# Kernel tuning notes

Measured on AMD Instinct MI355X. Metric: run time of the kernel, lower is better.

The kernel has to match this reference:

```python
import jax, jax.numpy as jnp
import numpy as np
from jax.scipy.special import logsumexp

L = 15      # DATA_MAX_SEG_LEN
K = 64      # XCRIBE_DIM
H = 16      # SEG_DIM
TAG = 32    # TAG_DIM
DUR = 4     # DURATION_DIM
NY = 15     # len(LABELS)
N = 16384   # sequence length
S = 2048    # number of gold segments
NEG = jnp.float32(-1e30)


def setup_inputs() -> dict:
    key = jax.random.key(0)
    ks = jax.random.split(key, 24)
    sL = 1.0 / np.sqrt(H)
    sV = 1.0 / np.sqrt(2 * H + TAG + DUR)
    sW = 1.0 / np.sqrt(H)

    def U(k, shape, s):
        return jax.random.uniform(k, shape, jnp.float32, -s, s)

    return dict(
        data=jax.random.normal(ks[0], (N, K), jnp.float32),
        fwd_Wih=U(ks[1], (4 * H, K), sL), fwd_Whh=U(ks[2], (4 * H, H), sL),
        fwd_bih=U(ks[3], (4 * H,), sL), fwd_bhh=U(ks[4], (4 * H,), sL),
        bwd_Wih=U(ks[5], (4 * H, K), sL), bwd_Whh=U(ks[6], (4 * H, H), sL),
        bwd_bih=U(ks[7], (4 * H,), sL), bwd_bhh=U(ks[8], (4 * H,), sL),
        fwd_h0=jax.random.normal(ks[9], (H,), jnp.float32),
        fwd_c0=jax.random.normal(ks[10], (H,), jnp.float32),
        bwd_h0=jax.random.normal(ks[11], (H,), jnp.float32),
        bwd_c0=jax.random.normal(ks[12], (H,), jnp.float32),
        Y_enc=jax.random.normal(ks[13], (NY, TAG), jnp.float32),
        Z_enc=jax.random.normal(ks[14], (L, DUR), jnp.float32),
        V_W=U(ks[15], (H, 2 * H + TAG + DUR), sV), V_b=U(ks[16], (H,), sV),
        W_W=U(ks[17], (1, H), sW), W_b=U(ks[18], (1,), sW),
        tags=jax.random.randint(ks[19], (S,), 0, NY),
        lengths=jax.random.randint(ks[20], (S,), 1, L + 1),
    )


def _lstm(xs, Wih, Whh, bih, bhh, h0, c0):
    # xs: [L, B, K] -> hidden outputs [L, B, H]; torch gate order i,f,g,o
    B = xs.shape[1]
    b = bih + bhh

    def step(carry, x):
        h, c = carry
        g = x @ Wih.T + h @ Whh.T + b
        i, f, gg, o = jnp.split(g, 4, axis=-1)
        c = jax.nn.sigmoid(f) * c + jax.nn.sigmoid(i) * jnp.tanh(gg)
        h = jax.nn.sigmoid(o) * jnp.tanh(c)
        return (h, c), h

    init = (jnp.broadcast_to(h0, (B, H)), jnp.broadcast_to(c0, (B, H)))
    _, hs = jax.lax.scan(step, init, xs)
    return hs


def reference(data, fwd_Wih, fwd_Whh, fwd_bih, fwd_bhh, fwd_h0, fwd_c0,
              bwd_Wih, bwd_Whh, bwd_bih, bwd_bhh, bwd_h0, bwd_c0,
              Y_enc, Z_enc, V_W, V_b, W_W, W_b, tags, lengths):
    n = data.shape[0]
    pos = jnp.arange(n)[:, None]      # [N,1]
    dd = jnp.arange(L)[None, :]       # [1,L]
    idx_f = jnp.minimum(pos + dd, n - 1)   # forward window indices
    idx_b = pos - dd                       # backward window indices (may be <0)

    win_f = data[idx_f].transpose(1, 0, 2)                  # [L,N,K]
    win_b = data[jnp.maximum(idx_b, 0)].transpose(1, 0, 2)  # [L,N,K]

    # fwd[i,d] = forward_precalc[i][i+d]; bwd[e,d] = backward_precalc[e-d][e]
    fwd = _lstm(win_f, fwd_Wih, fwd_Whh, fwd_bih, fwd_bhh, fwd_h0, fwd_c0).transpose(1, 0, 2)
    bwd = _lstm(win_b, bwd_Wih, bwd_Whh, bwd_bih, bwd_bhh, bwd_h0, bwd_c0).transpose(1, 0, 2)

    # gather fwd at (start=e-d, duration index d) -> aligned with end position e
    fwd_g = fwd[jnp.maximum(idx_b, 0), dd]          # [N,L,H]
    fb = jnp.concatenate([fwd_g, bwd], axis=-1)     # [N,L,2H]

    # split V across concat blocks: [fwd,bwd | Y | Z]
    V1 = V_W[:, :2 * H]; V2 = V_W[:, 2 * H:2 * H + TAG]; V3 = V_W[:, 2 * H + TAG:]
    base = fb @ V1.T + (Z_enc @ V3.T)[None, :, :] + V_b      # [N,L,H]
    ypart = Y_enc @ V2.T                                     # [NY,H]
    pre = base[:, :, None, :] + ypart[None, None, :, :]      # [N,L,NY,H]
    scores = jnp.tanh(pre) @ W_W[0] + W_b[0]                 # [N,L,NY]

    valid = idx_b >= 0
    A = jnp.where(valid, logsumexp(scores, axis=-1), NEG)    # [N,L] lse over labels

    # semi-Markov forward DP: log_alpha[i] = lse_d(log_alpha[i-d] + A[i-1,d-1])
    def dp(hist, a):  # hist[k] = log_alpha[i-1-k]
        new = logsumexp(hist + a)
        return jnp.concatenate([new[None], hist[:-1]]), new

    hist0 = jnp.full((L,), NEG, jnp.float32).at[0].set(0.0)
    _, alphas = jax.lax.scan(dp, hist0, A)
    logZ = alphas[-1]

    # gold-segment score; original never advances `chars`, so start is always 0
    gv = lengths < L
    gscores = scores[lengths - 1, lengths - 1, tags]
    indiv = jnp.sum(jnp.where(gv, gscores, 0.0))
    return logZ - indiv
```

## Files before the change

kernel.cpp:

```cpp
#include <hip/hip_runtime.h>

#define NPOS 16384
#define NEG  (-1e30f)

#define OFF_FWDH  0
#define OFF_BWDH  1966080
#define OFF_A     3932160
#define OFF_T0    4194304
#define OFF_R     4251904
#define OFF_GSC   4255504
#define OFF_CTR   4255744

struct Params {
    const float *data, *fWih, *fWhh, *fbih, *fbhh, *bWih, *bWhh, *bbih, *bbhh;
    const float *h0f, *c0f, *h0b, *c0b, *Yenc, *Zenc, *VW, *Vb, *WW, *Wb;
    const int *tags, *lengths;
    float *ws; float *out;
};

typedef _Float16 half2_t __attribute__((ext_vector_type(2)));

__device__ __forceinline__ half2_t u2h(unsigned int v) {
    return __builtin_bit_cast(half2_t, v);
}
__device__ __forceinline__ unsigned int packh(float a, float b) {
    half2_t h = { (_Float16)a, (_Float16)b };
    return __builtin_bit_cast(unsigned int, h);
}
__device__ __forceinline__ float fdot2_(unsigned int w, unsigned int x, float acc) {
    return __builtin_amdgcn_fdot2(u2h(w), u2h(x), acc, false);
}
__device__ __forceinline__ float sigf(float x) {
    return __builtin_amdgcn_rcpf(1.0f + __expf(-x));
}
__device__ __forceinline__ float tanhf_(float x) {
    return 1.0f - 2.0f * __builtin_amdgcn_rcpf(1.0f + __expf(2.0f * x));
}
__device__ __forceinline__ float lse15(const float* tv) {
    float a0 = fmaxf(tv[0], tv[1]),  a1 = fmaxf(tv[2], tv[3]);
    float a2 = fmaxf(tv[4], tv[5]),  a3 = fmaxf(tv[6], tv[7]);
    float a4 = fmaxf(tv[8], tv[9]),  a5 = fmaxf(tv[10], tv[11]);
    float a6 = fmaxf(tv[12], tv[13]);
    float b0 = fmaxf(a0, a1), b1 = fmaxf(a2, a3), b2 = fmaxf(a4, a5), b3 = fmaxf(a6, tv[14]);
    float mx = fmaxf(fmaxf(b0, b1), fmaxf(b2, b3));
    float e[15];
    #pragma unroll
    for (int i = 0; i < 15; i++) e[i] = __expf(tv[i] - mx);
    float s0 = e[0]+e[1], s1 = e[2]+e[3], s2 = e[4]+e[5], s3 = e[6]+e[7];
    float s4 = e[8]+e[9], s5 = e[10]+e[11], s6 = e[12]+e[13];
    float t0 = s0+s1, t1 = s2+s3, t2 = s4+s5, t3 = s6+e[14];
    return mx + __logf((t0+t1) + (t2+t3));
}

__device__ __forceinline__ void lse_mm(const float* src, float* dst, int nprod,
                                       int tid, int nthr)
{
    const int tot = nprod * 225;
    for (int e = tid; e < tot; e += nthr) {
        const int m = e / 225;
        const int r = e - m * 225;
        const int i = r / 15;
        const int j = r - i * 15;
        const float* Ar = src + (2*m + 1)*240 + i*16;
        const float* Bc = src + (2*m)*240 + j;
        float tv[15];
        #pragma unroll
        for (int k = 0; k < 15; k++) tv[k] = Ar[k] + Bc[k*16];
        dst[m*240 + i*16 + j] = lse15(tv);
    }
}

__global__ __launch_bounds__(512) void kA(Params p)
{
    __shared__ unsigned int xs2[78*33];
    __shared__ float xgT[64*78];
    __shared__ unsigned int hsh[2*512];
    __shared__ unsigned int wqx[2048];
    __shared__ unsigned int wqh[512];
    __shared__ float bq[64];

    const int tid  = threadIdx.x;
    const int lane = tid & 63;
    const int wq   = __builtin_amdgcn_readfirstlane(tid >> 6);
    const int dir  = blockIdx.y;
    const int P0   = blockIdx.x << 6;
    const int dbase = P0 - (dir ? 14 : 0);

    if (blockIdx.x == 0 && dir == 0 && tid == 0)
        ((unsigned int*)(p.ws + OFF_CTR))[0] = 0;

    const float* Wih = dir ? p.bWih : p.fWih;
    const float* Whh = dir ? p.bWhh : p.fWhh;
    const float* bih = dir ? p.bbih : p.fbih;
    const float* bhh = dir ? p.bbhh : p.fbhh;
    const float* h0  = dir ? p.h0b  : p.h0f;
    const float* c0  = dir ? p.c0b  : p.c0f;

    for (int e = tid; e < 2048; e += 512) {
        int k2 = e >> 6, pi = e & 63;
        int w = pi >> 3, jj = pi & 7;
        int j = ((jj >> 1) << 4) + 2*w + (jj & 1);
        wqx[e] = packh(Wih[j*64 + 2*k2], Wih[j*64 + 2*k2 + 1]);
    }
    if (tid < 512) {
        int m2 = tid >> 6, pi = tid & 63;
        int w = pi >> 3, jj = pi & 7;
        int j = ((jj >> 1) << 4) + 2*w + (jj & 1);
        wqh[tid] = packh(Whh[j*16 + 2*m2], Whh[j*16 + 2*m2 + 1]);
    }
    if (tid < 64) {
        int w = tid >> 3, jj = tid & 7;
        int j = ((jj >> 1) << 4) + 2*w + (jj & 1);
        bq[tid] = bih[j] + bhh[j];
    }
    for (int idx = tid; idx < 78*32; idx += 512) {
        int r = idx >> 5, c = idx & 31;
        int q = dbase + r;
        q = q < 0 ? 0 : (q > NPOS-1 ? NPOS-1 : q);
        float2 x2 = *(const float2*)(p.data + (size_t)q*64 + c*2);
        xs2[r*33 + c] = packh(x2.x, x2.y);
    }
    if (tid < 512) {
        int m2 = tid >> 6;
        hsh[tid] = packh(h0[2*m2], h0[2*m2 + 1]);
    }
    __syncthreads();

    #pragma unroll
    for (int pass = 0; pass < 2; pass++) {
        int r = pass*64 + lane;
        if (r < 78) {
            float acc[8];
            #pragma unroll
            for (int jj = 0; jj < 8; jj++) acc[jj] = bq[wq*8 + jj];
            #pragma unroll 8
            for (int k2 = 0; k2 < 32; k2++) {
                unsigned int xp = xs2[r*33 + k2];
                uint4 w0 = *(const uint4*)&wqx[k2*64 + wq*8];
                uint4 w1 = *(const uint4*)&wqx[k2*64 + wq*8 + 4];
                acc[0] = fdot2_(w0.x, xp, acc[0]);
                acc[1] = fdot2_(w0.y, xp, acc[1]);
                acc[2] = fdot2_(w0.z, xp, acc[2]);
                acc[3] = fdot2_(w0.w, xp, acc[3]);
                acc[4] = fdot2_(w1.x, xp, acc[4]);
                acc[5] = fdot2_(w1.y, xp, acc[5]);
                acc[6] = fdot2_(w1.z, xp, acc[6]);
                acc[7] = fdot2_(w1.w, xp, acc[7]);
            }
            #pragma unroll
            for (int jj = 0; jj < 8; jj++) xgT[(wq*8 + jj)*78 + r] = acc[jj];
        }
    }
    float cv0 = c0[wq*2], cv1 = c0[wq*2 + 1];
    unsigned int* outH = (unsigned int*)(p.ws + (dir ? OFF_BWDH : OFF_FWDH));
    __syncthreads();

    int buf = 0;
    for (int d = 0; d < 15; d++) {
        const int row = dir ? (lane + 14 - d) : (lane + d);
        float part[8];
        #pragma unroll
        for (int jj = 0; jj < 8; jj++) part[jj] = xgT[(wq*8 + jj)*78 + row];
        #pragma unroll
        for (int m2 = 0; m2 < 8; m2++) {
            unsigned int hp = hsh[buf*512 + m2*64 + lane];
            uint4 w0 = *(const uint4*)&wqh[m2*64 + wq*8];
            uint4 w1 = *(const uint4*)&wqh[m2*64 + wq*8 + 4];
            part[0] = fdot2_(w0.x, hp, part[0]);
            part[1] = fdot2_(w0.y, hp, part[1]);
            part[2] = fdot2_(w0.z, hp, part[2]);
            part[3] = fdot2_(w0.w, hp, part[3]);
            part[4] = fdot2_(w1.x, hp, part[4]);
            part[5] = fdot2_(w1.y, hp, part[5]);
            part[6] = fdot2_(w1.z, hp, part[6]);
            part[7] = fdot2_(w1.w, hp, part[7]);
        }
        float cn0 = sigf(part[2])*cv0 + sigf(part[0])*tanhf_(part[4]);
        float cn1 = sigf(part[3])*cv1 + sigf(part[1])*tanhf_(part[5]);
        cv0 = cn0; cv1 = cn1;
        float h0v = sigf(part[6])*tanhf_(cn0);
        float h1v = sigf(part[7])*tanhf_(cn1);
        unsigned int pk = packh(h0v, h1v);
        hsh[(buf^1)*512 + wq*64 + lane] = pk;
        outH[((size_t)d*NPOS + P0 + lane)*8 + wq] = pk;
        __syncthreads();
        buf ^= 1;
    }
}

__global__ __launch_bounds__(1024) void kBC(Params p)
{
    __shared__ float As[64*17];
    __shared__ unsigned int VWh[256];
    __shared__ float zbl[240];
    __shared__ float EY[240];
    __shared__ float Ms[16*240];
    __shared__ float Mp[8*240];
    const int tid = threadIdx.x;
    const int P0  = blockIdx.x << 6;
    float* ws = p.ws;

    if (tid < 240) {
        int y = tid >> 4, h = tid & 15;
        float acc = 0.f;
        for (int t = 0; t < 32; t++) acc += p.Yenc[y*32 + t] * p.VW[h*68 + 32 + t];
        EY[tid] = __expf(acc + acc);
        float z = p.Vb[h];
        for (int u = 0; u < 4; u++) z += p.Zenc[y*4 + u] * p.VW[h*68 + 64 + u];
        zbl[tid] = z;
    }
    if (tid < 256) {
        int h = tid >> 4, j2 = tid & 15;
        int col = (j2 < 8) ? 2*j2 : 16 + 2*(j2 - 8);
        VWh[tid] = packh(p.VW[h*68 + col], p.VW[h*68 + col + 1]);
    }
    __syncthreads();

    const int pl = tid & 63;
    const int d  = tid >> 6;
    const int pp = P0 + pl;
    float Aval = NEG;
    if (d < 15 && pp >= d) {
        const uint4* fptr = (const uint4*)((const unsigned int*)(ws + OFF_FWDH)
                            + ((size_t)d*NPOS + (pp - d))*8);
        const uint4* bptr = (const uint4*)((const unsigned int*)(ws + OFF_BWDH)
                            + ((size_t)d*NPOS + pp)*8);
        uint4 f0 = fptr[0], f1 = fptr[1];
        uint4 b0 = bptr[0], b1 = bptr[1];
        unsigned int fp_[8] = {f0.x, f0.y, f0.z, f0.w, f1.x, f1.y, f1.z, f1.w};
        unsigned int bp_[8] = {b0.x, b0.y, b0.z, b0.w, b1.x, b1.y, b1.z, b1.w};
        float E[16], w2[16], wsum = 0.f;
        #pragma unroll
        for (int h = 0; h < 16; h++) {
            float acc = zbl[d*16 + h];
            uint4 va = *(const uint4*)&VWh[h*16];
            uint4 vb = *(const uint4*)&VWh[h*16 + 4];
            uint4 vc = *(const uint4*)&VWh[h*16 + 8];
            uint4 vd = *(const uint4*)&VWh[h*16 + 12];
            acc = fdot2_(va.x, fp_[0], acc); acc = fdot2_(va.y, fp_[1], acc);
            acc = fdot2_(va.z, fp_[2], acc); acc = fdot2_(va.w, fp_[3], acc);
            acc = fdot2_(vb.x, fp_[4], acc); acc = fdot2_(vb.y, fp_[5], acc);
            acc = fdot2_(vb.z, fp_[6], acc); acc = fdot2_(vb.w, fp_[7], acc);
            acc = fdot2_(vc.x, bp_[0], acc); acc = fdot2_(vc.y, bp_[1], acc);
            acc = fdot2_(vc.z, bp_[2], acc); acc = fdot2_(vc.w, bp_[3], acc);
            acc = fdot2_(vd.x, bp_[4], acc); acc = fdot2_(vd.y, bp_[5], acc);
            acc = fdot2_(vd.z, bp_[6], acc); acc = fdot2_(vd.w, bp_[7], acc);
            E[h] = __expf(acc + acc);
            float w = p.WW[h];
            w2[h] = -2.0f * w;
            wsum += w;
        }
        const float cst = p.Wb[0] + wsum;
        float sc[15];
        #pragma unroll
        for (int y = 0; y < 15; y++) {
            float a = 0.f;
            #pragma unroll
            for (int h = 0; h < 16; h++)
                a = fmaf(w2[h], __builtin_amdgcn_rcpf(1.0f + E[h]*EY[y*16 + h]), a);
            sc[y] = cst + a;
        }
        Aval = lse15(sc);
        if (pp == d && pp < 15) {
            float* gsc = ws + OFF_GSC;
            #pragma unroll
            for (int y = 0; y < 15; y++) gsc[pp*15 + y] = sc[y];
        }
    }
    As[pl*17 + d] = Aval;
    __syncthreads();

    {
        const int wv = tid >> 6;
        const int ln = tid & 63;
        if (ln < 15) {
            float s[15];
            #pragma unroll
            for (int i = 0; i < 15; i++) s[i] = (i == ln) ? 0.f : NEG;
            const int t0 = wv * 4;
            #pragma unroll
            for (int q = 0; q < 4; q++) {
                const int t = t0 + q;
                float tv[15];
                #pragma unroll
                for (int i = 0; i < 15; i++) tv[i] = s[i] + As[t*17 + i];
                float nw = lse15(tv);
                #pragma unroll
                for (int i = 14; i > 0; i--) s[i] = s[i-1];
                s[0] = nw;
            }
            #pragma unroll
            for (int i = 0; i < 15; i++) Ms[wv*240 + i*16 + ln] = s[i];
        }
    }
    __syncthreads();

    lse_mm(Ms, Mp, 8, tid, 1024);  __syncthreads();
    lse_mm(Mp, Ms, 4, tid, 1024);  __syncthreads();
    lse_mm(Ms, Mp, 2, tid, 1024);  __syncthreads();
    if (tid < 225) {
        const int i = tid / 15, j = tid - (tid / 15) * 15;
        float tv[15];
        #pragma unroll
        for (int k = 0; k < 15; k++) tv[k] = Mp[240 + i*16 + k] + Mp[k*16 + j];
        (ws + OFF_T0)[blockIdx.x*225 + i*15 + j] = lse15(tv);
    }
}

__global__ __launch_bounds__(1024) void kDE(Params p)
{
    __shared__ float RA[16*240];
    __shared__ float RP[8*240];
    __shared__ float red[16];
    __shared__ float logZsh;
    __shared__ int lastFlag;
    const int tid = threadIdx.x;
    const int b   = blockIdx.x;
    unsigned int* ctr = (unsigned int*)(p.ws + OFF_CTR);

    {
        const float* T0 = p.ws + OFF_T0;
        for (int idx = tid; idx < 16*225; idx += 1024) {
            int t = idx / 225, r = idx - t*225;
            RA[t*240 + (r/15)*16 + (r%15)] = T0[(b*16 + t)*225 + r];
        }
        __syncthreads();
        lse_mm(RA, RP, 8, tid, 1024); __syncthreads();
        lse_mm(RP, RA, 4, tid, 1024); __syncthreads();
        lse_mm(RA, RP, 2, tid, 1024); __syncthreads();
        if (tid < 225) {
            const int i = tid / 15, j = tid - (tid / 15) * 15;
            float tv[15];
            #pragma unroll
            for (int k = 0; k < 15; k++) tv[k] = RP[240 + i*16 + k] + RP[k*16 + j];
            p.ws[OFF_R + b*225 + i*15 + j] = lse15(tv);
        }
    }
    __syncthreads();
    __threadfence();
    if (tid == 0) {
        unsigned int old = __hip_atomic_fetch_add(&ctr[0], 1u, __ATOMIC_ACQ_REL,
                                                  __HIP_MEMORY_SCOPE_AGENT);
        lastFlag = (old == 15u);
    }
    __syncthreads();
    if (!lastFlag) return;
    __threadfence();

    {
        const float* Rg = p.ws + OFF_R;
        for (int idx = tid; idx < 16*225; idx += 1024) {
            int t = idx / 225, r = idx - t*225;
            RA[t*240 + (r/15)*16 + (r%15)] = Rg[t*225 + r];
        }
        __syncthreads();
        lse_mm(RA, RP, 8, tid, 1024); __syncthreads();
        lse_mm(RP, RA, 4, tid, 1024); __syncthreads();
        lse_mm(RA, RP, 2, tid, 1024); __syncthreads();
        if (tid == 0) {
            float tv[15];
            #pragma unroll
            for (int k = 0; k < 15; k++) tv[k] = RP[240 + k] + RP[k*16];
            logZsh = lse15(tv);
        }
        const float* gsc = p.ws + OFF_GSC;
        float loc = 0.f;
        for (int s = tid; s < 2048; s += 1024) {
            int len = p.lengths[s];
            if (len < 15) loc += gsc[(len-1)*15 + p.tags[s]];
        }
        #pragma unroll
        for (int off = 32; off > 0; off >>= 1) loc += __shfl_down(loc, off);
        if ((tid & 63) == 0) red[tid >> 6] = loc;
        __syncthreads();
        if (tid == 0) {
            float ind = 0.f;
            #pragma unroll
            for (int q = 0; q < 16; q++) ind += red[q];
            p.out[0] = logZsh - ind;
        }
    }
}

extern "C" void kernel_launch(void* const* d_in, const int* in_sizes, int n_in,
                              void* d_out, int out_size, void* d_ws, size_t ws_size,
                              hipStream_t stream)
{
    Params prm;
    prm.data = (const float*)d_in[0];
    prm.fWih = (const float*)d_in[1];
    prm.fWhh = (const float*)d_in[2];
    prm.fbih = (const float*)d_in[3];
    prm.fbhh = (const float*)d_in[4];
    prm.bWih = (const float*)d_in[5];
    prm.bWhh = (const float*)d_in[6];
    prm.bbih = (const float*)d_in[7];
    prm.bbhh = (const float*)d_in[8];
    prm.h0f  = (const float*)d_in[9];
    prm.c0f  = (const float*)d_in[10];
    prm.h0b  = (const float*)d_in[11];
    prm.c0b  = (const float*)d_in[12];
    prm.Yenc = (const float*)d_in[13];
    prm.Zenc = (const float*)d_in[14];
    prm.VW   = (const float*)d_in[15];
    prm.Vb   = (const float*)d_in[16];
    prm.WW   = (const float*)d_in[17];
    prm.Wb   = (const float*)d_in[18];
    prm.tags    = (const int*)d_in[19];
    prm.lengths = (const int*)d_in[20];
    prm.ws  = (float*)d_ws;
    prm.out = (float*)d_out;

    hipLaunchKernelGGL(kA,  dim3(256, 2), dim3(512),  0, stream, prm);
    hipLaunchKernelGGL(kBC, dim3(256),    dim3(1024), 0, stream, prm);
    hipLaunchKernelGGL(kDE, dim3(16),     dim3(1024), 0, stream, prm);
}
```

Measured before the change: 170.7 us.

## Fold final semiring reduction into kBC with atomic last-block tree

Removes the third kernel launch by performing the two-level log-semiring matrix reduction inside kBC, using per-group atomic counters so the last block of each 16-block group reduces that group, and a second counter so the last group reduces to logZ. Gold-segment scores are kept in shared memory in block 0, which also computes the individual score sum. This is meant to remove one launch and its gap, at the cost of extra fences and atomics plus serialized tail work in the last-arriving blocks.

```diff
diff --git a/kernel.cpp b/kernel.cpp
--- a/kernel.cpp
+++ b/kernel.cpp
@@ -10,6 +10,7 @@
 #define OFF_R     4251904
 #define OFF_GSC   4255504
 #define OFF_CTR   4255744
+#define OFF_IND   4255776
 
 struct Params {
     const float *data, *fWih, *fWhh, *fbih, *fbhh, *bWih, *bWhh, *bbih, *bbhh;
@@ -86,8 +87,8 @@
     const int P0   = blockIdx.x << 6;
     const int dbase = P0 - (dir ? 14 : 0);
 
-    if (blockIdx.x == 0 && dir == 0 && tid == 0)
-        ((unsigned int*)(p.ws + OFF_CTR))[0] = 0;
+    if (blockIdx.x == 0 && dir == 0 && tid < 17)
+        ((unsigned int*)(p.ws + OFF_CTR))[tid] = 0;
 
     const float* Wih = dir ? p.bWih : p.fWih;
     const float* Whh = dir ? p.bWhh : p.fWhh;
@@ -196,9 +197,13 @@
     __shared__ float EY[240];
     __shared__ float Ms[16*240];
     __shared__ float Mp[8*240];
+    __shared__ float gscL[240];
+    __shared__ float red[16];
+    __shared__ int flagS;
     const int tid = threadIdx.x;
     const int P0  = blockIdx.x << 6;
     float* ws = p.ws;
+    unsigned int* ctr = (unsigned int*)(ws + OFF_CTR);
 
     if (tid < 240) {
         int y = tid >> 4, h = tid & 15;
@@ -262,9 +267,8 @@
         }
         Aval = lse15(sc);
         if (pp == d && pp < 15) {
-            float* gsc = ws + OFF_GSC;
-            #pragma unroll
-            for (int y = 0; y < 15; y++) gsc[pp*15 + y] = sc[y];
+            #pragma unroll
+            for (int y = 0; y < 15; y++) gscL[pp*16 + y] = sc[y];
         }
     }
     As[pl*17 + d] = Aval;
@@ -305,69 +309,12 @@
         for (int k = 0; k < 15; k++) tv[k] = Mp[240 + i*16 + k] + Mp[k*16 + j];
         (ws + OFF_T0)[blockIdx.x*225 + i*15 + j] = lse15(tv);
     }
-}
-
-__global__ __launch_bounds__(1024) void kDE(Params p)
-{
-    __shared__ float RA[16*240];
-    __shared__ float RP[8*240];
-    __shared__ float red[16];
-    __shared__ float logZsh;
-    __shared__ int lastFlag;
-    const int tid = threadIdx.x;
-    const int b   = blockIdx.x;
-    unsigned int* ctr = (unsigned int*)(p.ws + OFF_CTR);
-
-    {
-        const float* T0 = p.ws + OFF_T0;
-        for (int idx = tid; idx < 16*225; idx += 1024) {
-            int t = idx / 225, r = idx - t*225;
-            RA[t*240 + (r/15)*16 + (r%15)] = T0[(b*16 + t)*225 + r];
-        }
-        __syncthreads();
-        lse_mm(RA, RP, 8, tid, 1024); __syncthreads();
-        lse_mm(RP, RA, 4, tid, 1024); __syncthreads();
-        lse_mm(RA, RP, 2, tid, 1024); __syncthreads();
-        if (tid < 225) {
-            const int i = tid / 15, j = tid - (tid / 15) * 15;
-            float tv[15];
-            #pragma unroll
-            for (int k = 0; k < 15; k++) tv[k] = RP[240 + i*16 + k] + RP[k*16 + j];
-            p.ws[OFF_R + b*225 + i*15 + j] = lse15(tv);
-        }
-    }
-    __syncthreads();
-    __threadfence();
-    if (tid == 0) {
-        unsigned int old = __hip_atomic_fetch_add(&ctr[0], 1u, __ATOMIC_ACQ_REL,
-                                                  __HIP_MEMORY_SCOPE_AGENT);
-        lastFlag = (old == 15u);
-    }
-    __syncthreads();
-    if (!lastFlag) return;
-    __threadfence();
-
-    {
-        const float* Rg = p.ws + OFF_R;
-        for (int idx = tid; idx < 16*225; idx += 1024) {
-            int t = idx / 225, r = idx - t*225;
-            RA[t*240 + (r/15)*16 + (r%15)] = Rg[t*225 + r];
-        }
-        __syncthreads();
-        lse_mm(RA, RP, 8, tid, 1024); __syncthreads();
-        lse_mm(RP, RA, 4, tid, 1024); __syncthreads();
-        lse_mm(RA, RP, 2, tid, 1024); __syncthreads();
-        if (tid == 0) {
-            float tv[15];
-            #pragma unroll
-            for (int k = 0; k < 15; k++) tv[k] = RP[240 + k] + RP[k*16];
-            logZsh = lse15(tv);
-        }
-        const float* gsc = p.ws + OFF_GSC;
+
+    if (blockIdx.x == 0) {
         float loc = 0.f;
         for (int s = tid; s < 2048; s += 1024) {
             int len = p.lengths[s];
-            if (len < 15) loc += gsc[(len-1)*15 + p.tags[s]];
+            if (len < 15) loc += gscL[(len-1)*16 + p.tags[s]];
         }
         #pragma unroll
         for (int off = 32; off > 0; off >>= 1) loc += __shfl_down(loc, off);
@@ -377,7 +324,68 @@
             float ind = 0.f;
             #pragma unroll
             for (int q = 0; q < 16; q++) ind += red[q];
-            p.out[0] = logZsh - ind;
+            ws[OFF_IND] = ind;
+        }
+    }
+
+    const int g = blockIdx.x >> 4;
+    __syncthreads();
+    __threadfence();
+    if (tid == 0) {
+        unsigned int old = __hip_atomic_fetch_add(&ctr[g], 1u, __ATOMIC_ACQ_REL,
+                                                  __HIP_MEMORY_SCOPE_AGENT);
+        flagS = (old == 15u);
+    }
+    __syncthreads();
+    if (!flagS) return;
+    __threadfence();
+
+    {
+        const float* T0 = ws + OFF_T0;
+        for (int idx = tid; idx < 16*225; idx += 1024) {
+            int t = idx / 225, r = idx - t*225;
+            Ms[t*240 + (r/15)*16 + (r%15)] = T0[((g<<4) + t)*225 + r];
+        }
+        __syncthreads();
+        lse_mm(Ms, Mp, 8, tid, 1024); __syncthreads();
+        lse_mm(Mp, Ms, 4, tid, 1024); __syncthreads();
+        lse_mm(Ms, Mp, 2, tid, 1024); __syncthreads();
+        if (tid < 225) {
+            const int i = tid / 15, j = tid - (tid / 15) * 15;
+            float tv[15];
+            #pragma unroll
+            for (int k = 0; k < 15; k++) tv[k] = Mp[240 + i*16 + k] + Mp[k*16 + j];
+            ws[OFF_R + g*225 + i*15 + j] = lse15(tv);
+        }
+    }
+
+    __syncthreads();
+    __threadfence();
+    if (tid == 0) {
+        unsigned int old = __hip_atomic_fetch_add(&ctr[16], 1u, __ATOMIC_ACQ_REL,
+                                                  __HIP_MEMORY_SCOPE_AGENT);
+        flagS = (old == 15u);
+    }
+    __syncthreads();
+    if (!flagS) return;
+    __threadfence();
+
+    {
+        const float* Rg = ws + OFF_R;
+        for (int idx = tid; idx < 16*225; idx += 1024) {
+            int t = idx / 225, r = idx - t*225;
+            Ms[t*240 + (r/15)*16 + (r%15)] = Rg[t*225 + r];
+        }
+        __syncthreads();
+        lse_mm(Ms, Mp, 8, tid, 1024); __syncthreads();
+        lse_mm(Mp, Ms, 4, tid, 1024); __syncthreads();
+        lse_mm(Ms, Mp, 2, tid, 1024); __syncthreads();
+        if (tid == 0) {
+            float tv[15];
+            #pragma unroll
+            for (int k = 0; k < 15; k++) tv[k] = Mp[240 + k] + Mp[k*16];
+            float logZ = lse15(tv);
+            p.out[0] = logZ - ws[OFF_IND];
         }
     }
 }
@@ -413,5 +421,4 @@
 
     hipLaunchKernelGGL(kA,  dim3(256, 2), dim3(512),  0, stream, prm);
     hipLaunchKernelGGL(kBC, dim3(256),    dim3(1024), 0, stream, prm);
-    hipLaunchKernelGGL(kDE, dim3(16),     dim3(1024), 0, stream, prm);
-}
+}
```

Measured after the change: 252.6 us. 48.0% more time.
